# Optimization experiments

Measured on AMD Instinct MI355X. Metric: run time of the kernel, lower is better.

## Reference

```python
import jax, jax.numpy as jnp
import numpy as np

NUM_ANGLES = 120
MAX_CONF = 100
FIELD = 50  # prot_field_size L


def setup_inputs() -> dict:
    key = jax.random.key(0)
    ks = jax.random.split(key, 4)
    B = 16
    return {
        "receptor": jax.random.normal(ks[0], (B, 1, FIELD, FIELD), jnp.float32),
        "ligand": jax.random.normal(ks[1], (B, 1, FIELD, FIELD), jnp.float32),
        "w_repr": jax.random.normal(ks[2], (2, 1, 3, 3), jnp.float32) * 0.3,
        "b_repr": jnp.zeros((2,), jnp.float32),
        "w_score": jax.random.normal(ks[3], (1, 4), jnp.float32) * 0.1,
        "b_score": jnp.zeros((1,), jnp.float32),
    }


def reference(receptor, ligand, w_repr, b_repr, w_score, b_score):
    B, _, H, W = receptor.shape  # H = W = FIELD

    # ---- scoring_model.repr : conv(1->2, SAME) + ReLU (stand-in for EQ repr net)
    def repr_net(x):
        y = jax.lax.conv_general_dilated(
            x, w_repr, (1, 1), "SAME", dimension_numbers=("NCHW", "OIHW", "NCHW"))
        return jax.nn.relu(y + b_repr[None, :, None, None])

    rec_feat = repr_net(receptor)  # (B,2,H,W)
    lig_feat = repr_net(ligand)    # (B,2,H,W)

    # ---- rotate: torch affine_grid + grid_sample (bilinear, align_corners=True, zero pad)
    ang = (2.0 * np.pi / NUM_ANGLES) * jnp.arange(NUM_ANGLES, dtype=jnp.float32)
    ca, sa = jnp.cos(ang), jnp.sin(ang)
    lin = jnp.linspace(-1.0, 1.0, H)
    gy, gx = jnp.meshgrid(lin, lin, indexing="ij")  # rows=y, cols=x
    # theta = [[c,-s,0],[s,c,0]] maps output coords -> input coords
    x_in = ca[:, None, None] * gx - sa[:, None, None] * gy  # (A,H,W)
    y_in = sa[:, None, None] * gx + ca[:, None, None] * gy
    px = (x_in + 1.0) * 0.5 * (W - 1)
    py = (y_in + 1.0) * 0.5 * (H - 1)
    x0 = jnp.floor(px).astype(jnp.int32); y0 = jnp.floor(py).astype(jnp.int32)
    x1 = x0 + 1; y1 = y0 + 1
    wx1 = px - x0; wx0 = 1.0 - wx1
    wy1 = py - y0; wy0 = 1.0 - wy1

    def tap(yi, xi, wgt):
        val = lig_feat[:, :, jnp.clip(yi, 0, H - 1), jnp.clip(xi, 0, W - 1)]  # (B,C,A,H,W)
        ok = ((yi >= 0) & (yi < H) & (xi >= 0) & (xi < W)).astype(lig_feat.dtype)
        return val * (wgt * ok)

    lig_rot = (tap(y0, x0, wy0 * wx0) + tap(y0, x1, wy0 * wx1)
               + tap(y1, x0, wy1 * wx0) + tap(y1, x1, wy1 * wx1))
    lig_rot = jnp.transpose(lig_rot, (2, 0, 1, 3, 4))  # (A,B,C,H,W)

    # ---- ProteinConv2D: FFT cross-correlation over all channel pairs, output 2L x 2L
    S = 2 * H
    pad = ((0, 0), (0, 0), (0, H), (0, W))
    Frec = jnp.fft.rfft2(jnp.pad(rec_feat, pad))              # (B,C,S,S/2+1)
    Flig = jnp.fft.rfft2(jnp.pad(lig_rot, ((0, 0),) + pad))   # (A,B,C,S,S/2+1)
    cross = jnp.einsum("bcxy,abdxy->abcdxy", jnp.conj(Frec), Flig)
    A_, C = NUM_ANGLES, rec_feat.shape[1]
    corr = jnp.fft.irfft2(cross.reshape(A_, B, C * C, S, S // 2 + 1), s=(S, S))
    corr = jnp.fft.fftshift(corr, axes=(-2, -1))              # (A,B,4,S,S) centered

    # ---- scoring_model.scorer : Linear(4->1) applied per translation
    scores = jnp.einsum("abcij,c->abij", corr, w_score[0]) + b_score[0]  # (A,B,S,S)

    # ---- update_top: greedy iterative argmin extraction with zero masking
    flat = scores.reshape(A_, B, S * S)

    def greedy(v):
        def step(s, _):
            i = jnp.argmin(s)
            return s.at[i].set(0.0), (i, s[i])
        _, (idx, val) = jax.lax.scan(step, v, None, length=MAX_CONF)
        return idx, val

    idxs, vals = jax.vmap(jax.vmap(greedy))(flat)  # each (A,B,K)

    # ---- final top-1 per batch over all angles/extractions (stable first-min tiebreak)
    K = MAX_CONF
    vals_b = jnp.transpose(vals, (1, 0, 2)).reshape(B, A_ * K)
    j = jnp.argmin(vals_b, axis=1)
    a = j // K
    k = j % K
    pos = idxs[a, jnp.arange(B), k]
    Lf = jnp.float32(S / 2)
    x = (pos // S).astype(jnp.float32)
    y = (pos % S).astype(jnp.float32)
    angles_out = ang[a][:, None]                               # (B,1)
    translations = jnp.stack([x - Lf, y - Lf], axis=1)         # (B,2)
    return angles_out, translations
```

## Files before the change

### kernel.cpp

```cpp
#include <hip/hip_runtime.h>
#include <math.h>

#define NANG 120
#define NB   16
#define H    50
#define SD   100
#define NBIN 51
#define PADB 7
#define BROWS 69
#define BST  106
#define WST  104
#define RTST 52
#define CLAG 104
#define AX   58

__device__ __align__(16) float g_Arec[NB*2*AX*NBIN*2 + 64];
__device__ __align__(16) float g_ligc[NB*2*H*H];
__device__ __align__(16) float g_W[H*WST];
__device__ __align__(16) float g_P[NBIN*128 + 64];
__device__ __align__(16) float g_C[(size_t)NANG*NB*2*NBIN*CLAG/ NBIN * NBIN];
__device__ float g_resV[NANG*NB];
__device__ int   g_resP[NANG*NB];

__device__ const int g_s8[8][2] = {
  {-1,127},{-9,47},{7,-49},{-17,39},{15,-41},{-25,31},{23,-33},{127,127}
};

__global__ __launch_bounds__(512) void k_prep(const float* __restrict__ rec,
                                              const float* __restrict__ lig,
                                              const float* __restrict__ wr,
                                              const float* __restrict__ br,
                                              const float* __restrict__ wsc) {
  const int blk = blockIdx.x;
  const int tid = threadIdx.x;
  if (blk == NB) {
    for (int u = tid; u < H*WST; u += 512) {
      int y = u / WST, col = u % WST;
      float v = 0.f;
      if (col < 2*NBIN) {
        int om = col >> 1;
        int k = (om * y) % SD;
        double ang = 6.283185307179586 * (double)k / 100.0;
        v = (col & 1) ? (float)(-sin(ang)) : (float)cos(ang);
      }
      g_W[u] = v;
    }
    for (int u = tid; u < NBIN*128; u += 512) {
      int om = u >> 7, q = u & 127;
      int dy = q >> 1;
      float v = 0.f;
      if (dy <= 49) {
        int k = (om * dy) % SD;
        double ang = 6.283185307179586 * (double)k / 100.0;
        v = (q & 1) ? (float)sin(ang) : (float)cos(ang);
      }
      g_P[u] = v;
    }
    return;
  }
  const int b = blk;
  __shared__ float recf[2*H*H];
  __shared__ float tbl[SD*2];
  for (int k = tid; k < SD; k += 512) {
    double ang = 6.283185307179586 * (double)k / 100.0;
    tbl[2*k]   = (float)cos(ang);
    tbl[2*k+1] = (float)sin(ang);
  }
  const float* rimg = rec + b*H*H;
  const float* limg = lig + b*H*H;
  for (int p = tid; p < H*H; p += 512) {
    int i = p / H, j = p - (p/H)*H;
    float ar0 = br[0], ar1 = br[1], al0 = br[0], al1 = br[1];
    for (int di = 0; di < 3; ++di) {
      int ii = i + di - 1;
      if (ii < 0 || ii >= H) continue;
      for (int dj = 0; dj < 3; ++dj) {
        int jj = j + dj - 1;
        if (jj < 0 || jj >= H) continue;
        float rv = rimg[ii*H+jj], lv = limg[ii*H+jj];
        float w0 = wr[di*3 + dj], w1 = wr[9 + di*3 + dj];
        ar0 += w0*rv; ar1 += w1*rv; al0 += w0*lv; al1 += w1*lv;
      }
    }
    ar0 = fmaxf(ar0, 0.f); ar1 = fmaxf(ar1, 0.f);
    al0 = fmaxf(al0, 0.f); al1 = fmaxf(al1, 0.f);
    recf[p] = ar0; recf[H*H + p] = ar1;
    g_ligc[((b*2+0)*H + i)*H + j] = wsc[0]*al0 + wsc[1]*al1;
    g_ligc[((b*2+1)*H + i)*H + j] = wsc[2]*al0 + wsc[3]*al1;
  }
  for (int u = tid; u < 2*8*102; u += 512) {
    int c = u / 816; int r = u % 816;
    int x = 50 + r / 102; int q = r % 102;
    g_Arec[((b*2+c)*AX + x)*102 + q] = 0.f;
  }
  __syncthreads();
  for (int u = tid; u < 2*H*NBIN; u += 512) {
    int om = u % NBIN; int rest = u / NBIN; int x = rest % H; int c = rest / H;
    const float* row = recf + (c*H + x)*H;
    float sr = 0.f, si = 0.f;
    int k = 0;
    for (int y = 0; y < H; ++y) {
      float rv = row[y];
      sr += rv * tbl[2*k];
      si -= rv * tbl[2*k+1];
      k += om; if (k >= SD) k -= SD;
    }
    float* dst = g_Arec + ((b*2+c)*AX + x)*102 + 2*om;
    dst[0] = sr; dst[1] = si;
  }
}

#define STEP8(uu) do { \
  float Ar = ar_[(uu)&7], Ai = ai_[(uu)&7]; \
  { const int sl=(uu)&7;     cr0 += Ar*br_[sl]+Ai*bi_[sl]; ci0 += Ar*bi_[sl]-Ai*br_[sl]; } \
  { const int sl=((uu)+1)&7; cr1 += Ar*br_[sl]+Ai*bi_[sl]; ci1 += Ar*bi_[sl]-Ai*br_[sl]; } \
  { const int sl=((uu)+2)&7; cr2 += Ar*br_[sl]+Ai*bi_[sl]; ci2 += Ar*bi_[sl]-Ai*br_[sl]; } \
  { const int sl=((uu)+3)&7; cr3 += Ar*br_[sl]+Ai*bi_[sl]; ci3 += Ar*bi_[sl]-Ai*br_[sl]; } \
  { const int sl=((uu)+4)&7; cr4 += Ar*br_[sl]+Ai*bi_[sl]; ci4 += Ar*bi_[sl]-Ai*br_[sl]; } \
  { const int sl=((uu)+5)&7; cr5 += Ar*br_[sl]+Ai*bi_[sl]; ci5 += Ar*bi_[sl]-Ai*br_[sl]; } \
  { const int sl=((uu)+6)&7; cr6 += Ar*br_[sl]+Ai*bi_[sl]; ci6 += Ar*bi_[sl]-Ai*br_[sl]; } \
  { const int sl=((uu)+7)&7; cr7 += Ar*br_[sl]+Ai*bi_[sl]; ci7 += Ar*bi_[sl]-Ai*br_[sl]; } \
} while(0)

#define TILE8(D0) do { \
  const int d0 = (D0); \
  const int x_lo = max(0, -(d0+7)); \
  const int x_hi = min(H, H - d0); \
  const int ng = (x_hi - x_lo + 7) >> 3; \
  float cr0=0,cr1=0,cr2=0,cr3=0,cr4=0,cr5=0,cr6=0,cr7=0; \
  float ci0=0,ci1=0,ci2=0,ci3=0,ci4=0,ci5=0,ci6=0,ci7=0; \
  _Pragma("unroll 1") \
  for (int c = 0; c < 2; ++c) { \
    const float* Ap = g_Arec + ((b*2+c)*AX + x_lo)*102 + 2*om; \
    const float* Bp = sB + c*(BROWS*BST) + (PADB + x_lo + d0)*BST + 2*om; \
    float br_[8], bi_[8], ar_[8], ai_[8]; \
    _Pragma("unroll") \
    for (int s = 0; s < 8; ++s) { \
      float2 bv = *(const float2*)&Bp[s*BST]; \
      br_[s] = bv.x; bi_[s] = bv.y; \
      float2 av = *(const float2*)&Ap[s*102]; \
      ar_[s] = av.x; ai_[s] = av.y; \
    } \
    _Pragma("unroll 1") \
    for (int g = 0; g < ng-1; ++g) { \
      _Pragma("unroll") \
      for (int u = 0; u < 8; ++u) { \
        STEP8(u); \
        float2 bv = *(const float2*)&Bp[(u+8)*BST]; \
        br_[u] = bv.x; bi_[u] = bv.y; \
        float2 av = *(const float2*)&Ap[(u+8)*102]; \
        ar_[u] = av.x; ai_[u] = av.y; \
      } \
      Bp += 8*BST; Ap += 8*102; \
    } \
    _Pragma("unroll") \
    for (int u = 0; u < 8; ++u) { \
      STEP8(u); \
      if (u < 7) { \
        float2 bv = *(const float2*)&Bp[(u+8)*BST]; \
        br_[u] = bv.x; bi_[u] = bv.y; \
      } \
    } \
  } \
  if (omValid) { \
    const float sc = (om == 0 || om == 50) ? 0.5f : 1.0f; \
    float* dst = g_C + (size_t)bid*10608 + om*CLAG + (d0 + 49); \
    float4 v0 = {cr0*sc, cr1*sc, cr2*sc, cr3*sc}; \
    float4 v1 = {cr4*sc, cr5*sc, cr6*sc, cr7*sc}; \
    float4 w0 = {ci0*sc, ci1*sc, ci2*sc, ci3*sc}; \
    float4 w1 = {ci4*sc, ci5*sc, ci6*sc, ci7*sc}; \
    *(float4*)&dst[0] = v0; *(float4*)&dst[4] = v1; \
    *(float4*)&dst[5304] = w0; *(float4*)&dst[5308] = w1; \
  } \
} while(0)

__global__ __launch_bounds__(512, 4) void k_main() {
  const int bid = blockIdx.x;
  const int a = bid % NANG;
  const int b = bid / NANG;
  const int tid = threadIdx.x;

  __shared__ __align__(16) float sMem[19844];
  float* sB  = sMem;
  float* Rt0 = sMem + 14628;
  float* Rt1 = sMem + 17228;
  float* Cr  = sMem;
  float* Ci  = sMem + 5304;
  float* sRedV = sMem + 19828;
  int*   sRedP = (int*)(sMem + 19836);

  for (int u = tid; u < 2*19*BST; u += 512) {
    int ch = u / (19*BST);
    int r  = (u % (19*BST)) / BST;
    int col = u % BST;
    int row = (r < PADB) ? r : r + 50;
    sB[ch*(BROWS*BST) + row*BST + col] = 0.f;
  }

  float angf = 0.05235987755982988f * (float)a;
  float ca = cosf(angf), sa = sinf(angf);
  const float* L0 = g_ligc + (b*2+0)*H*H;
  const float* L1 = g_ligc + (b*2+1)*H*H;
  for (int p = tid; p < H*H; p += 512) {
    int i = p / H, j = p - (p/H)*H;
    float gy = -1.f + (float)i*(2.f/49.f);
    float gx = -1.f + (float)j*(2.f/49.f);
    float x_in = ca*gx - sa*gy;
    float y_in = sa*gx + ca*gy;
    float px = (x_in + 1.f)*0.5f*49.f;
    float py = (y_in + 1.f)*0.5f*49.f;
    float fx = floorf(px), fy = floorf(py);
    int x0 = (int)fx, y0 = (int)fy;
    int x1 = x0 + 1, y1 = y0 + 1;
    float wx1 = px - fx, wx0 = 1.f - wx1;
    float wy1 = py - fy, wy0 = 1.f - wy1;
    float v0 = 0.f, v1 = 0.f;
    if (y0 >= 0 && y0 < H) {
      if (x0 >= 0 && x0 < H) { float w = wy0*wx0; int o = y0*H+x0; v0 += w*L0[o]; v1 += w*L1[o]; }
      if (x1 >= 0 && x1 < H) { float w = wy0*wx1; int o = y0*H+x1; v0 += w*L0[o]; v1 += w*L1[o]; }
    }
    if (y1 >= 0 && y1 < H) {
      if (x0 >= 0 && x0 < H) { float w = wy1*wx0; int o = y1*H+x0; v0 += w*L0[o]; v1 += w*L1[o]; }
      if (x1 >= 0 && x1 < H) { float w = wy1*wx1; int o = y1*H+x1; v0 += w*L0[o]; v1 += w*L1[o]; }
    }
    Rt0[j*RTST + i] = v0;
    Rt1[j*RTST + i] = v1;
  }
  __syncthreads();

  if (tid < 442) {
    int c = tid / 221;
    int r = tid % 221;
    int cg = r % 17;
    int it = r / 17;
    int i0 = it*4;
    int col0 = 6*cg;
    float pacc[4][6];
    #pragma unroll
    for (int p = 0; p < 4; ++p)
      #pragma unroll
      for (int q = 0; q < 6; ++q) pacc[p][q] = 0.f;
    const float* rtc = Rt0 + c*(H*RTST) + i0;
    const float* wt = g_W + col0;
    #pragma unroll 2
    for (int y = 0; y < H; ++y) {
      float4 rv = *(const float4*)&rtc[y*RTST];
      float ww[6];
      #pragma unroll
      for (int q = 0; q < 3; ++q) {
        float2 w2 = *(const float2*)&wt[y*WST + 2*q];
        ww[2*q] = w2.x; ww[2*q+1] = w2.y;
      }
      float rr[4] = {rv.x, rv.y, rv.z, rv.w};
      #pragma unroll
      for (int p = 0; p < 4; ++p)
        #pragma unroll
        for (int q = 0; q < 6; ++q) pacc[p][q] += rr[p]*ww[q];
    }
    float* dst = sB + c*(BROWS*BST) + col0;
    #pragma unroll
    for (int p = 0; p < 4; ++p) {
      int i = i0 + p;
      if (i < H) {
        #pragma unroll
        for (int q = 0; q < 3; ++q) {
          float2 o = {pacc[p][2*q], pacc[p][2*q+1]};
          *(float2*)&dst[(PADB+i)*BST + 2*q] = o;
        }
      }
    }
  }
  __syncthreads();

  const int wid = tid >> 6, lane = tid & 63;
  const int om = (lane <= 50) ? lane : 50;
  const bool omValid = (lane <= 50);
  const int d0A = g_s8[wid][0];
  const int d0B = g_s8[wid][1];

  if (d0A != 127) { TILE8(d0A); }
  if (d0B != 127) { TILE8(d0B); }
  __syncthreads();

  {
    const float4* src = (const float4*)(g_C + (size_t)bid*10608);
    float4* dst = (float4*)sMem;
    for (int u = tid; u < 2652; u += 512) dst[u] = src[u];
  }
  __syncthreads();

  float bestV = 3.0e38f; int bestP = 0;
  if (tid < 442) {
    int lt = tid % 26;
    int dt = tid / 26;
    int l0 = 4*lt, dy0 = 3*dt;
    float su[4][3], sv[4][3];
    #pragma unroll
    for (int k = 0; k < 4; ++k)
      #pragma unroll
      for (int j = 0; j < 3; ++j) { su[k][j] = 0.f; sv[k][j] = 0.f; }
    const float* crp = Cr + l0;
    const float* cip = Ci + l0;
    const float* tp = g_P + 2*dy0;
    #pragma unroll 3
    for (int om2 = 0; om2 < NBIN; ++om2) {
      float4 c4 = *(const float4*)&crp[om2*CLAG];
      float4 i4 = *(const float4*)&cip[om2*CLAG];
      float2 t0 = *(const float2*)&tp[om2*128];
      float2 t1 = *(const float2*)&tp[om2*128 + 2];
      float2 t2 = *(const float2*)&tp[om2*128 + 4];
      float cc[4] = {c4.x, c4.y, c4.z, c4.w};
      float ii[4] = {i4.x, i4.y, i4.z, i4.w};
      float co[3] = {t0.x, t1.x, t2.x};
      float si[3] = {t0.y, t1.y, t2.y};
      #pragma unroll
      for (int k = 0; k < 4; ++k)
        #pragma unroll
        for (int j = 0; j < 3; ++j) {
          su[k][j] += cc[k]*co[j];
          sv[k][j] += ii[k]*si[j];
        }
    }
    #pragma unroll
    for (int k = 0; k < 4; ++k) {
      int lagIdx = l0 + k;
      if (lagIdx <= 98) {
        int row = lagIdx + 1;
        #pragma unroll
        for (int j = 0; j < 3; ++j) {
          int dy = dy0 + j;
          if (dy <= 49) {
            float vp = su[k][j] - sv[k][j];
            float vm = su[k][j] + sv[k][j];
            int posp = row*SD + (50 + dy);
            int posm = row*SD + (50 - dy);
            if (vp < bestV || (vp == bestV && posp < bestP)) { bestV = vp; bestP = posp; }
            if (vm < bestV || (vm == bestV && posm < bestP)) { bestV = vm; bestP = posm; }
          }
        }
      }
    }
  }

  #pragma unroll
  for (int off = 32; off > 0; off >>= 1) {
    float v2 = __shfl_xor(bestV, off, 64);
    int   p2 = __shfl_xor(bestP, off, 64);
    if (v2 < bestV || (v2 == bestV && p2 < bestP)) { bestV = v2; bestP = p2; }
  }
  if (lane == 0) { sRedV[wid] = bestV; sRedP[wid] = bestP; }
  __syncthreads();
  if (tid == 0) {
    float bv = sRedV[0]; int bp = sRedP[0];
    for (int w = 1; w < 8; ++w) {
      float v2 = sRedV[w]; int p2 = sRedP[w];
      if (v2 < bv || (v2 == bv && p2 < bp)) { bv = v2; bp = p2; }
    }
    g_resV[bid] = bv; g_resP[bid] = bp;
  }
}

__global__ void k_final(float* __restrict__ out) {
  int b = threadIdx.x;
  if (b >= NB) return;
  float bv = 0.f; int bp = 0; int ba = 0;
  for (int a = 0; a < NANG; ++a) {
    float v = g_resV[b*NANG + a];
    if (v < bv) { bv = v; bp = g_resP[b*NANG + a]; ba = a; }
  }
  out[b] = 0.05235987755982988f * (float)ba;
  out[NB + 2*b]     = (float)(bp / SD) - 50.f;
  out[NB + 2*b + 1] = (float)(bp % SD) - 50.f;
}

extern "C" void kernel_launch(void* const* d_in, const int* in_sizes, int n_in,
                              void* d_out, int out_size, void* d_ws, size_t ws_size,
                              hipStream_t stream) {
  const float* rec = (const float*)d_in[0];
  const float* lig = (const float*)d_in[1];
  const float* wr  = (const float*)d_in[2];
  const float* br  = (const float*)d_in[3];
  const float* wsc = (const float*)d_in[4];
  (void)in_sizes; (void)n_in; (void)out_size; (void)d_ws; (void)ws_size;
  hipLaunchKernelGGL(k_prep, dim3(NB+1), dim3(512), 0, stream, rec, lig, wr, br, wsc);
  hipLaunchKernelGGL(k_main, dim3(NANG*NB), dim3(512), 0, stream);
  hipLaunchKernelGGL(k_final, dim3(1), dim3(64), 0, stream, (float*)d_out);
}
```

Measured before the change: 295.7 us.

## Keep real correlation in LDS, shrink global staging, split prep, atomic top-1 key

The real part of the per-block correlation spectrum now stays in shared memory. Only the imaginary part goes through global memory, and the lag stride is cut from 104 to 100. The phase table g_P is copied into LDS, the prep kernel splits the DFT frequencies across four blocks per batch, and the final argmin uses a packed 64-bit atomicMin key instead of a per-block result array. These changes aim to cut global traffic, raise prep parallelism and remove a block-level reduction sync. The risks are that the CrL region overlaps Rt buffers while TILE8 runs, and that the key encoding must reproduce the original first-min tie-break.

```diff
diff --git a/kernel.cpp b/kernel.cpp
--- a/kernel.cpp
+++ b/kernel.cpp
@@ -11,16 +11,15 @@
 #define BST  106
 #define WST  104
 #define RTST 52
-#define CLAG 104
+#define CLAG 100
 #define AX   58
 
 __device__ __align__(16) float g_Arec[NB*2*AX*NBIN*2 + 64];
 __device__ __align__(16) float g_ligc[NB*2*H*H];
 __device__ __align__(16) float g_W[H*WST];
 __device__ __align__(16) float g_P[NBIN*128 + 64];
-__device__ __align__(16) float g_C[(size_t)NANG*NB*2*NBIN*CLAG/ NBIN * NBIN];
-__device__ float g_resV[NANG*NB];
-__device__ int   g_resP[NANG*NB];
+__device__ __align__(16) float g_C[(size_t)NANG*NB*5100];
+__device__ unsigned long long g_key[NB];
 
 __device__ const int g_s8[8][2] = {
   {-1,127},{-9,47},{7,-49},{-17,39},{15,-41},{-25,31},{23,-33},{127,127}
@@ -33,7 +32,7 @@
                                               const float* __restrict__ wsc) {
   const int blk = blockIdx.x;
   const int tid = threadIdx.x;
-  if (blk == NB) {
+  if (blk == NB*4) {
     for (int u = tid; u < H*WST; u += 512) {
       int y = u / WST, col = u % WST;
       float v = 0.f;
@@ -56,9 +55,13 @@
       }
       g_P[u] = v;
     }
+    for (int i = tid; i < NB; i += 512) g_key[i] = (0x80000000ULL << 21);
     return;
   }
-  const int b = blk;
+  const int b = blk >> 2;
+  const int part = blk & 3;
+  const int omBase = part * 13;
+  const int nOm = (part == 3) ? 12 : 13;
   __shared__ float recf[2*H*H];
   __shared__ float tbl[SD*2];
   for (int k = tid; k < SD; k += 512) {
@@ -83,19 +86,24 @@
       }
     }
     ar0 = fmaxf(ar0, 0.f); ar1 = fmaxf(ar1, 0.f);
-    al0 = fmaxf(al0, 0.f); al1 = fmaxf(al1, 0.f);
     recf[p] = ar0; recf[H*H + p] = ar1;
-    g_ligc[((b*2+0)*H + i)*H + j] = wsc[0]*al0 + wsc[1]*al1;
-    g_ligc[((b*2+1)*H + i)*H + j] = wsc[2]*al0 + wsc[3]*al1;
-  }
-  for (int u = tid; u < 2*8*102; u += 512) {
-    int c = u / 816; int r = u % 816;
-    int x = 50 + r / 102; int q = r % 102;
-    g_Arec[((b*2+c)*AX + x)*102 + q] = 0.f;
+    if (part == 0) {
+      al0 = fmaxf(al0, 0.f); al1 = fmaxf(al1, 0.f);
+      g_ligc[((b*2+0)*H + i)*H + j] = wsc[0]*al0 + wsc[1]*al1;
+      g_ligc[((b*2+1)*H + i)*H + j] = wsc[2]*al0 + wsc[3]*al1;
+    }
+  }
+  if (part == 0) {
+    for (int u = tid; u < 2*8*102; u += 512) {
+      int c = u / 816; int r = u % 816;
+      int x = 50 + r / 102; int q = r % 102;
+      g_Arec[((b*2+c)*AX + x)*102 + q] = 0.f;
+    }
   }
   __syncthreads();
-  for (int u = tid; u < 2*H*NBIN; u += 512) {
-    int om = u % NBIN; int rest = u / NBIN; int x = rest % H; int c = rest / H;
+  for (int u = tid; u < 2*H*nOm; u += 512) {
+    int om = omBase + u % nOm;
+    int rest = u / nOm; int x = rest % H; int c = rest / H;
     const float* row = recf + (c*H + x)*H;
     float sr = 0.f, si = 0.f;
     int k = 0;
@@ -164,13 +172,19 @@
   } \
   if (omValid) { \
     const float sc = (om == 0 || om == 50) ? 0.5f : 1.0f; \
-    float* dst = g_C + (size_t)bid*10608 + om*CLAG + (d0 + 49); \
+    const int base = om*CLAG + (d0 + 49); \
+    float* crl = CrL + base; \
+    float* gci = g_C + (size_t)bid*5100 + base; \
     float4 v0 = {cr0*sc, cr1*sc, cr2*sc, cr3*sc}; \
-    float4 v1 = {cr4*sc, cr5*sc, cr6*sc, cr7*sc}; \
     float4 w0 = {ci0*sc, ci1*sc, ci2*sc, ci3*sc}; \
-    float4 w1 = {ci4*sc, ci5*sc, ci6*sc, ci7*sc}; \
-    *(float4*)&dst[0] = v0; *(float4*)&dst[4] = v1; \
-    *(float4*)&dst[5304] = w0; *(float4*)&dst[5308] = w1; \
+    *(float4*)&crl[0] = v0; \
+    *(float4*)&gci[0] = w0; \
+    if (d0 != 47) { \
+      float4 v1 = {cr4*sc, cr5*sc, cr6*sc, cr7*sc}; \
+      float4 w1 = {ci4*sc, ci5*sc, ci6*sc, ci7*sc}; \
+      *(float4*)&crl[4] = v1; \
+      *(float4*)&gci[4] = w1; \
+    } \
   } \
 } while(0)
 
@@ -180,14 +194,13 @@
   const int b = bid / NANG;
   const int tid = threadIdx.x;
 
-  __shared__ __align__(16) float sMem[19844];
+  __shared__ __align__(16) float sMem[19828];
   float* sB  = sMem;
   float* Rt0 = sMem + 14628;
   float* Rt1 = sMem + 17228;
-  float* Cr  = sMem;
-  float* Ci  = sMem + 5304;
-  float* sRedV = sMem + 19828;
-  int*   sRedP = (int*)(sMem + 19836);
+  float* CrL = sMem + 14628;
+  float* CiL = sMem;
+  float* sP  = sMem + 5100;
 
   for (int u = tid; u < 2*19*BST; u += 512) {
     int ch = u / (19*BST);
@@ -283,32 +296,36 @@
   __syncthreads();
 
   {
-    const float4* src = (const float4*)(g_C + (size_t)bid*10608);
-    float4* dst = (float4*)sMem;
-    for (int u = tid; u < 2652; u += 512) dst[u] = src[u];
+    const float4* src = (const float4*)(g_C + (size_t)bid*5100);
+    float4* dst = (float4*)CiL;
+    for (int u = tid; u < 1275; u += 512) dst[u] = src[u];
+    for (int u = tid; u < 51*50; u += 512) {
+      int o = u / 50, q2 = (u % 50)*2;
+      *(float2*)&sP[o*100 + q2] = *(const float2*)&g_P[o*128 + q2];
+    }
   }
   __syncthreads();
 
   float bestV = 3.0e38f; int bestP = 0;
-  if (tid < 442) {
-    int lt = tid % 26;
-    int dt = tid / 26;
+  if (tid < 425) {
+    int lt = tid % 25;
+    int dt = tid / 25;
     int l0 = 4*lt, dy0 = 3*dt;
     float su[4][3], sv[4][3];
     #pragma unroll
     for (int k = 0; k < 4; ++k)
       #pragma unroll
       for (int j = 0; j < 3; ++j) { su[k][j] = 0.f; sv[k][j] = 0.f; }
-    const float* crp = Cr + l0;
-    const float* cip = Ci + l0;
-    const float* tp = g_P + 2*dy0;
+    const float* crp = CrL + l0;
+    const float* cip = CiL + l0;
+    const float* tp = sP + 2*dy0;
     #pragma unroll 3
     for (int om2 = 0; om2 < NBIN; ++om2) {
       float4 c4 = *(const float4*)&crp[om2*CLAG];
       float4 i4 = *(const float4*)&cip[om2*CLAG];
-      float2 t0 = *(const float2*)&tp[om2*128];
-      float2 t1 = *(const float2*)&tp[om2*128 + 2];
-      float2 t2 = *(const float2*)&tp[om2*128 + 4];
+      float2 t0 = *(const float2*)&tp[om2*100];
+      float2 t1 = *(const float2*)&tp[om2*100 + 2];
+      float2 t2 = *(const float2*)&tp[om2*100 + 4];
       float cc[4] = {c4.x, c4.y, c4.z, c4.w};
       float ii[4] = {i4.x, i4.y, i4.z, i4.w};
       float co[3] = {t0.x, t1.x, t2.x};
@@ -348,29 +365,25 @@
     int   p2 = __shfl_xor(bestP, off, 64);
     if (v2 < bestV || (v2 == bestV && p2 < bestP)) { bestV = v2; bestP = p2; }
   }
-  if (lane == 0) { sRedV[wid] = bestV; sRedP[wid] = bestP; }
-  __syncthreads();
-  if (tid == 0) {
-    float bv = sRedV[0]; int bp = sRedP[0];
-    for (int w = 1; w < 8; ++w) {
-      float v2 = sRedV[w]; int p2 = sRedP[w];
-      if (v2 < bv || (v2 == bv && p2 < bp)) { bv = v2; bp = p2; }
-    }
-    g_resV[bid] = bv; g_resP[bid] = bp;
+  if (lane == 0) {
+    unsigned int u = __float_as_uint(bestV);
+    u = (u & 0x80000000u) ? ~u : (u | 0x80000000u);
+    unsigned long long key = ((unsigned long long)u << 21) |
+                             ((unsigned long long)(unsigned)a << 14) |
+                             (unsigned long long)(unsigned)bestP;
+    atomicMin(&g_key[b], key);
   }
 }
 
 __global__ void k_final(float* __restrict__ out) {
   int b = threadIdx.x;
   if (b >= NB) return;
-  float bv = 0.f; int bp = 0; int ba = 0;
-  for (int a = 0; a < NANG; ++a) {
-    float v = g_resV[b*NANG + a];
-    if (v < bv) { bv = v; bp = g_resP[b*NANG + a]; ba = a; }
-  }
-  out[b] = 0.05235987755982988f * (float)ba;
-  out[NB + 2*b]     = (float)(bp / SD) - 50.f;
-  out[NB + 2*b + 1] = (float)(bp % SD) - 50.f;
+  unsigned long long key = g_key[b];
+  int a   = (int)((key >> 14) & 127ULL);
+  int pos = (int)(key & 16383ULL);
+  out[b] = 0.05235987755982988f * (float)a;
+  out[NB + 2*b]     = (float)(pos / SD) - 50.f;
+  out[NB + 2*b + 1] = (float)(pos % SD) - 50.f;
 }
 
 extern "C" void kernel_launch(void* const* d_in, const int* in_sizes, int n_in,
@@ -382,7 +395,7 @@
   const float* br  = (const float*)d_in[3];
   const float* wsc = (const float*)d_in[4];
   (void)in_sizes; (void)n_in; (void)out_size; (void)d_ws; (void)ws_size;
-  hipLaunchKernelGGL(k_prep, dim3(NB+1), dim3(512), 0, stream, rec, lig, wr, br, wsc);
+  hipLaunchKernelGGL(k_prep, dim3(NB*4+1), dim3(512), 0, stream, rec, lig, wr, br, wsc);
   hipLaunchKernelGGL(k_main, dim3(NANG*NB), dim3(512), 0, stream);
   hipLaunchKernelGGL(k_final, dim3(1), dim3(64), 0, stream, (float*)d_out);
 }
```

Measured after the change: 279.3 us. 1.06x faster.
